# Performance work log

Measured on AMD Instinct MI355X. Metric: run time of the kernel, lower is better.

Reference implementation:

```python
import jax, jax.numpy as jnp
import numpy as np

B, T_IN, IN = 512, 64, 16
HS, OUT = 32, 32          # Seq2Seq hidden_size; decoder output_size == hidden_size
H = HS * 30               # actual GRU state width = 960
T_PRED = 48


def _p(key, shape, scale=0.05):
    return jax.random.normal(key, shape, dtype=jnp.float32) * scale


def setup_inputs() -> dict:
    key = jax.random.key(0)
    ks = jax.random.split(key, 24)
    G = 3 * H
    return {
        "in_data": jax.random.normal(ks[0], (B, T_IN, IN), dtype=jnp.float32),
        "last_location": jax.random.normal(ks[1], (B, 1, HS), dtype=jnp.float32),
        "pred_length": T_PRED,
        # encoder GRU (2 layers)
        "enc_Wih0": _p(ks[2], (G, IN)), "enc_Whh0": _p(ks[3], (G, H)),
        "enc_bih0": _p(ks[4], (G,)), "enc_bhh0": _p(ks[5], (G,)),
        "enc_Wih1": _p(ks[6], (G, H)), "enc_Whh1": _p(ks[7], (G, H)),
        "enc_bih1": _p(ks[8], (G,)), "enc_bhh1": _p(ks[9], (G,)),
        # decoder GRU (2 layers), input size = HS
        "dec_Wih0": _p(ks[10], (G, HS)), "dec_Whh0": _p(ks[11], (G, H)),
        "dec_bih0": _p(ks[12], (G,)), "dec_bhh0": _p(ks[13], (G,)),
        "dec_Wih1": _p(ks[14], (G, H)), "dec_Whh1": _p(ks[15], (G, H)),
        "dec_bih1": _p(ks[16], (G,)), "dec_bhh1": _p(ks[17], (G,)),
        # output projection H -> OUT
        "lin_W": _p(ks[18], (OUT, H)), "lin_b": _p(ks[19], (OUT,)),
    }


def gru_cell(x, h, Wih, Whh, bih, bhh):
    # PyTorch GRU cell convention (gate order: r, z, n)
    gi = x @ Wih.T + bih
    gh = h @ Whh.T + bhh
    ir, iz, inn = jnp.split(gi, 3, axis=-1)
    hr, hz, hn = jnp.split(gh, 3, axis=-1)
    r = jax.nn.sigmoid(ir + hr)
    z = jax.nn.sigmoid(iz + hz)
    n = jnp.tanh(inn + r * hn)
    return (1.0 - z) * n + z * h


def gru_layer(xs, Wih, Whh, bih, bhh):
    # xs: [T, B, in] time-major; zero initial state
    h0 = jnp.zeros((xs.shape[1], Whh.shape[1]), xs.dtype)
    def step(h, x):
        h2 = gru_cell(x, h, Wih, Whh, bih, bhh)
        return h2, h2
    hT, ys = jax.lax.scan(step, h0, xs)
    return ys, hT


def reference(in_data, last_location, pred_length,
              enc_Wih0, enc_Whh0, enc_bih0, enc_bhh0,
              enc_Wih1, enc_Whh1, enc_bih1, enc_bhh1,
              dec_Wih0, dec_Whh0, dec_bih0, dec_bhh0,
              dec_Wih1, dec_Whh1, dec_bih1, dec_bhh1,
              lin_W, lin_b):
    # ---- encoder: 2-layer GRU over in_data ----
    xs = jnp.transpose(in_data, (1, 0, 2))          # [T, B, IN]
    ys0, h0 = gru_layer(xs, enc_Wih0, enc_Whh0, enc_bih0, enc_bhh0)
    ys1, h1 = gru_layer(ys0, enc_Wih1, enc_Whh1, enc_bih1, enc_bhh1)

    x0 = last_location[:, 0, :]                      # [B, HS]

    def dec_step(carry, _):
        hl0, hl1, x = carry
        hl0 = gru_cell(x, hl0, dec_Wih0, dec_Whh0, dec_bih0, dec_bhh0)
        hl1 = gru_cell(hl0, hl1, dec_Wih1, dec_Whh1, dec_bih1, dec_bhh1)
        # dropout is identity in eval mode
        out = hl1 @ lin_W.T + lin_b                  # [B, OUT]
        hcat = jnp.concatenate([hl0, hl1], axis=-1)  # [B, 2H] (layer-major, as permute+view)
        return (hl0, hl1, out), (out, hcat)

    (_, _, _), (outs, hcats) = jax.lax.scan(dec_step, (h0, h1, x0), None, length=pred_length)
    outputs = jnp.transpose(outs, (1, 0, 2))         # [B, T_pred, OUT]
    hidden_outputs = jnp.transpose(hcats, (1, 0, 2)) # [B, T_pred, 2H]
    return outputs, hidden_outputs
```

## Files before the change

### kernel.cpp

```cpp
#include <hip/hip_runtime.h>
#include <cstdint>
#include <cstddef>

typedef __bf16 bf16;
typedef __bf16 bf16x8 __attribute__((ext_vector_type(8)));
typedef float f32x4 __attribute__((ext_vector_type(4)));

static __device__ __forceinline__ f32x4 mfma16(bf16x8 a, bf16x8 b, f32x4 c) {
  return __builtin_amdgcn_mfma_f32_16x16x32_bf16(a, b, c, 0, 0, 0);
}

struct StepArgs {
  const bf16* X;
  const bf16* Hb;
  const bf16* Wt;
  const float* bA;
  const float* bB;
  const float* Hf_prev;
  float* Hf_next;
  bf16* Hb_next;
  float* out_hidden;
  int ldx;
  int KXPAD;
  int Ktot;
  int _pad;
};

__global__ __launch_bounds__(256) void gru_step(StepArgs a0, StepArgs a1) {
  const StepArgs a = (blockIdx.z == 0) ? a0 : a1;
  const int id = blockIdx.x;
  const int gq = id >> 6, bm = (id >> 3) & 7, gr = id & 7;
  const int g = gq * 8 + gr;
  if (g >= 30) return;

  __shared__ bf16 ldsB[2 * 3840];

  const int tid = threadIdx.x;
  const int wv = tid >> 6, lane = tid & 63, col = lane & 15, quad = lane >> 4;
  const int mh = wv & 1, uh = wv >> 1;
  const int Ktot = a.Ktot, KXPAD = a.KXPAD;
  const int nb = tid >> 3, cc = tid & 7;

  const bf16* Wb0 = a.Wt + ((size_t)g * 96 + nb) * Ktot + cc * 4;
  const size_t WrS = (size_t)32 * Ktot;
  char* ldsW = (char*)ldsB + nb * 80 + cc * 8;

  const int rowA = bm * 64 + mh * 32 + col;
  const bf16* Xrow = a.X + (size_t)rowA * a.ldx + quad * 8;
  const bf16* Hrow = a.Hb + (size_t)rowA * 960 + quad * 8 - KXPAD;
  const int ldx16 = 16 * a.ldx;

  const f32x4 z4 = {0.f, 0.f, 0.f, 0.f};
  f32x4 acc[2][3] = {{z4, z4, z4}, {z4, z4, z4}};
  f32x4 ck0 = z4, ck1 = z4;

  uint2 br00, br01, br02, br10, br11, br12;
  bf16x8 ar0, ar1;

#define STAGE0(K) do { br00 = *(const uint2*)(Wb0 + (K)); \
                       br01 = *(const uint2*)(Wb0 + WrS + (K)); \
                       br02 = *(const uint2*)(Wb0 + 2 * WrS + (K)); } while (0)
#define STAGE1(K) do { br10 = *(const uint2*)(Wb0 + (K)); \
                       br11 = *(const uint2*)(Wb0 + WrS + (K)); \
                       br12 = *(const uint2*)(Wb0 + 2 * WrS + (K)); } while (0)
#define LOADA(K) do { int _k = (K); \
    if (_k < KXPAD) { const bf16* _p = Xrow + _k; ar0 = *(const bf16x8*)_p; ar1 = *(const bf16x8*)(_p + ldx16); } \
    else { const bf16* _p = Hrow + _k; ar0 = *(const bf16x8*)_p; ar1 = *(const bf16x8*)(_p + 16 * 960); } } while (0)

  const char* ldsRd = (char*)ldsB + (uh * 16 + col) * 80 + quad * 16;

#define GRU_ITER(PH) do { \
    if (k0 == KXPAD) { ck0 = acc[0][2]; ck1 = acc[1][2]; } \
    char* _d = ldsW + bufoff; \
    *(uint2*)_d = br##PH##0; \
    *(uint2*)(_d + 32 * 80) = br##PH##1; \
    *(uint2*)(_d + 64 * 80) = br##PH##2; \
    bf16x8 am0 = ar0, am1 = ar1; \
    __syncthreads(); \
    { int _k2 = k0 + 64; if (_k2 >= Ktot) _k2 = 0; STAGE##PH(_k2); } \
    { int _kn = k0 + 32; if (_kn >= Ktot) _kn = 0; LOADA(_kn); } \
    const char* _rp = ldsRd + bufoff; \
    _Pragma("unroll") \
    for (int gate = 0; gate < 3; ++gate) { \
      bf16x8 _bf = *(const bf16x8*)(_rp + gate * (32 * 80)); \
      acc[0][gate] = mfma16(am0, _bf, acc[0][gate]); \
      acc[1][gate] = mfma16(am1, _bf, acc[1][gate]); \
    } \
    k0 += 32; bufoff ^= 7680; \
  } while (0)

  STAGE0(0);
  STAGE1(32 < Ktot ? 32 : 0);
  LOADA(0);
  int k0 = 0, bufoff = 0;
  const int T = Ktot >> 5;
  for (int it = 0; it + 2 <= T; it += 2) {
    GRU_ITER(0);
    GRU_ITER(1);
  }
  if (T & 1) { GRU_ITER(0); }

#undef GRU_ITER
#undef STAGE0
#undef STAGE1
#undef LOADA

  const int uu = uh * 16 + col;
  const int u = g * 32 + uu;
  const int gbase = g * 96;
  const float bAr = a.bA[gbase + uu];
  const float bAz = a.bA[gbase + 32 + uu];
  const float bAn = a.bA[gbase + 64 + uu];
  const float bBn = a.bB[gbase + 64 + uu];
#pragma unroll
  for (int mf = 0; mf < 2; ++mf) {
    f32x4 R = acc[mf][0], Z = acc[mf][1], Nf = acc[mf][2];
    f32x4 Nx = mf ? ck1 : ck0;
    const int mbase = bm * 64 + mh * 32 + mf * 16 + quad * 4;
#pragma unroll
    for (int r = 0; r < 4; ++r) {
      const int mm = mbase + r;
      float rg = 1.f / (1.f + __expf(-(R[r] + bAr)));
      float zg = 1.f / (1.f + __expf(-(Z[r] + bAz)));
      float inn = Nx[r] + bAn;
      float hn = (Nf[r] - Nx[r]) + bBn;
      float ng = tanhf(fmaf(rg, hn, inn));
      float hold = a.Hf_prev[(size_t)mm * 960 + u];
      float hnew = fmaf(zg, hold - ng, ng);
      a.Hf_next[(size_t)mm * 960 + u] = hnew;
      a.Hb_next[(size_t)mm * 960 + u] = (bf16)hnew;
      if (a.out_hidden) a.out_hidden[(size_t)mm * 92160 + u] = hnew;
    }
  }
}

__global__ __launch_bounds__(256) void final_linear(const float* __restrict__ hid,
                                                    const bf16* __restrict__ Wb,
                                                    const float* __restrict__ bias,
                                                    float* __restrict__ outp) {
  const int tid = threadIdx.x;
  const int wv = tid >> 6, lane = tid & 63, col = lane & 15, quad = lane >> 4;
  const int row = blockIdx.x * 64 + wv * 16 + col;
  const int b = row / 48, t = row - b * 48;
  const float* arow = hid + (size_t)b * 92160 + (size_t)t * 1920 + 960 + quad * 8;
  const f32x4 z4 = {0.f, 0.f, 0.f, 0.f};
  f32x4 acc0 = z4, acc1 = z4;
  for (int k0 = 0; k0 < 960; k0 += 32) {
    f32x4 x0 = *(const f32x4*)(arow + k0);
    f32x4 x1 = *(const f32x4*)(arow + k0 + 4);
    bf16x8 af;
#pragma unroll
    for (int i = 0; i < 4; ++i) { af[i] = (bf16)x0[i]; af[4 + i] = (bf16)x1[i]; }
    bf16x8 b0 = *(const bf16x8*)(Wb + (size_t)col * 960 + k0 + quad * 8);
    bf16x8 b1 = *(const bf16x8*)(Wb + (size_t)(16 + col) * 960 + k0 + quad * 8);
    acc0 = mfma16(af, b0, acc0);
    acc1 = mfma16(af, b1, acc1);
  }
  const int mbase = blockIdx.x * 64 + wv * 16 + quad * 4;
#pragma unroll
  for (int r = 0; r < 4; ++r) {
    const int mm = mbase + r;
    const int b2 = mm / 48, t2 = mm - b2 * 48;
    float* o = outp + (size_t)b2 * 1536 + (size_t)t2 * 32;
    o[col] = acc0[r] + bias[col];
    o[16 + col] = acc1[r] + bias[16 + col];
  }
}

__global__ void prep_weight(const float* __restrict__ Wih, const float* __restrict__ Whh,
                            bf16* __restrict__ dst, int Kx, int KXPAD, int Ktot) {
  const int total = 2880 * Ktot;
  for (int e = blockIdx.x * blockDim.x + threadIdx.x; e < total; e += gridDim.x * blockDim.x) {
    int n = e / Ktot, k = e - n * Ktot;
    int g = n / 96, loc = n - g * 96, gate = loc >> 5, uu = loc & 31;
    int c = gate * 960 + g * 32 + uu;
    float v;
    if (k < KXPAD) v = (k < Kx) ? Wih[(size_t)c * Kx + k] : 0.f;
    else v = Whh[(size_t)c * 960 + (k - KXPAD)];
    dst[e] = (bf16)v;
  }
}

__global__ void prep_weight_dec0(const float* __restrict__ Wih, const float* __restrict__ Whh,
                                 const float* __restrict__ linW, bf16* __restrict__ dst) {
  const int total = 2880 * 1920;
  for (int e = blockIdx.x * blockDim.x + threadIdx.x; e < total; e += gridDim.x * blockDim.x) {
    int n = e / 1920, k = e - n * 1920;
    int g = n / 96, loc = n - g * 96, gate = loc >> 5, uu = loc & 31;
    int c = gate * 960 + g * 32 + uu;
    float v;
    if (k < 960) {
      float s = 0.f;
      for (int j = 0; j < 32; ++j) s = fmaf(Wih[(size_t)c * 32 + j], linW[(size_t)j * 960 + k], s);
      v = s;
    } else {
      v = Whh[(size_t)c * 960 + (k - 960)];
    }
    dst[e] = (bf16)v;
  }
}

__global__ void prep_bias(const float* __restrict__ bih, const float* __restrict__ bhh,
                          float* __restrict__ bA, float* __restrict__ bB) {
  int n = blockIdx.x * blockDim.x + threadIdx.x;
  if (n >= 2880) return;
  int g = n / 96, loc = n - g * 96, gate = loc >> 5, uu = loc & 31;
  int c = gate * 960 + g * 32 + uu;
  if (gate < 2) { bA[n] = bih[c] + bhh[c]; bB[n] = 0.f; }
  else          { bA[n] = bih[c];          bB[n] = bhh[c]; }
}

__global__ void prep_bias_dec0(const float* __restrict__ bih, const float* __restrict__ bhh,
                               const float* __restrict__ Wih, const float* __restrict__ linb,
                               float* __restrict__ bA, float* __restrict__ bB) {
  int n = blockIdx.x * blockDim.x + threadIdx.x;
  if (n >= 2880) return;
  int g = n / 96, loc = n - g * 96, gate = loc >> 5, uu = loc & 31;
  int c = gate * 960 + g * 32 + uu;
  float bi = bih[c];
  for (int j = 0; j < 32; ++j) bi = fmaf(Wih[(size_t)c * 32 + j], linb[j], bi);
  if (gate < 2) { bA[n] = bi + bhh[c]; bB[n] = 0.f; }
  else          { bA[n] = bi;          bB[n] = bhh[c]; }
}

__global__ void prep_xenc(const float* __restrict__ in_data, bf16* __restrict__ X) {
  int i = blockIdx.x * blockDim.x + threadIdx.x;
  if (i >= 64 * 512 * 32) return;
  int k = i & 31, m = (i >> 5) & 511, t = i >> 14;
  X[i] = (k < 16) ? (bf16)in_data[((size_t)m * 64 + t) * 16 + k] : (bf16)0.f;
}

__global__ void cvt_bf16(const float* __restrict__ s, bf16* __restrict__ d, int n) {
  int i = blockIdx.x * blockDim.x + threadIdx.x;
  if (i < n) d[i] = (bf16)s[i];
}

extern "C" void kernel_launch(void* const* d_in, const int* in_sizes, int n_in,
                              void* d_out, int out_size, void* d_ws, size_t ws_size,
                              hipStream_t stream) {
  (void)in_sizes; (void)n_in; (void)out_size; (void)ws_size;
  const float* in_data = (const float*)d_in[0];
  const float* last_loc = (const float*)d_in[1];
  const float* eWih0 = (const float*)d_in[3];
  const float* eWhh0 = (const float*)d_in[4];
  const float* ebih0 = (const float*)d_in[5];
  const float* ebhh0 = (const float*)d_in[6];
  const float* eWih1 = (const float*)d_in[7];
  const float* eWhh1 = (const float*)d_in[8];
  const float* ebih1 = (const float*)d_in[9];
  const float* ebhh1 = (const float*)d_in[10];
  const float* dWih0 = (const float*)d_in[11];
  const float* dWhh0 = (const float*)d_in[12];
  const float* dbih0 = (const float*)d_in[13];
  const float* dbhh0 = (const float*)d_in[14];
  const float* dWih1 = (const float*)d_in[15];
  const float* dWhh1 = (const float*)d_in[16];
  const float* dbih1 = (const float*)d_in[17];
  const float* dbhh1 = (const float*)d_in[18];
  const float* linW = (const float*)d_in[19];
  const float* linb = (const float*)d_in[20];
  float* outp = (float*)d_out;

  uint8_t* base = (uint8_t*)d_ws;
  size_t off = 0;
  auto alloc = [&](size_t bytes) -> void* {
    void* p = base + off;
    off += (bytes + 255) & ~(size_t)255;
    return p;
  };
  bf16* WtE0 = (bf16*)alloc(2880ull * 992 * 2);
  bf16* WtE1 = (bf16*)alloc(2880ull * 1920 * 2);
  bf16* WtD0a = (bf16*)alloc(2880ull * 992 * 2);
  bf16* WtD0 = (bf16*)alloc(2880ull * 1920 * 2);
  bf16* WtD1 = (bf16*)alloc(2880ull * 1920 * 2);
  bf16* linWb = (bf16*)alloc(32ull * 960 * 2);
  float* bA_e0 = (float*)alloc(2880 * 4); float* bB_e0 = (float*)alloc(2880 * 4);
  float* bA_e1 = (float*)alloc(2880 * 4); float* bB_e1 = (float*)alloc(2880 * 4);
  float* bA_d0a = (float*)alloc(2880 * 4); float* bB_d0a = (float*)alloc(2880 * 4);
  float* bA_d0 = (float*)alloc(2880 * 4); float* bB_d0 = (float*)alloc(2880 * 4);
  float* bA_d1 = (float*)alloc(2880 * 4); float* bB_d1 = (float*)alloc(2880 * 4);
  bf16* Xenc = (bf16*)alloc(64ull * 512 * 32 * 2);
  bf16* Xloc = (bf16*)alloc(512ull * 32 * 2);
  const int HS_ELEMS = 512 * 960;
  float* states = (float*)alloc((size_t)HS_ELEMS * (4 * 4 + 4 * 2));
  float* h0f[2] = {states, states + HS_ELEMS};
  float* h1f[2] = {states + 2 * HS_ELEMS, states + 3 * HS_ELEMS};
  bf16* bstates = (bf16*)(states + 4 * HS_ELEMS);
  bf16* h0b[2] = {bstates, bstates + HS_ELEMS};
  bf16* h1b[2] = {bstates + 2 * HS_ELEMS, bstates + 3 * HS_ELEMS};

  hipMemsetAsync(states, 0, (size_t)HS_ELEMS * (4 * 4 + 4 * 2), stream);
  prep_weight<<<4096, 256, 0, stream>>>(eWih0, eWhh0, WtE0, 16, 32, 992);
  prep_weight<<<8192, 256, 0, stream>>>(eWih1, eWhh1, WtE1, 960, 960, 1920);
  prep_weight<<<4096, 256, 0, stream>>>(dWih0, dWhh0, WtD0a, 32, 32, 992);
  prep_weight_dec0<<<8192, 256, 0, stream>>>(dWih0, dWhh0, linW, WtD0);
  prep_weight<<<8192, 256, 0, stream>>>(dWih1, dWhh1, WtD1, 960, 960, 1920);
  prep_bias<<<12, 256, 0, stream>>>(ebih0, ebhh0, bA_e0, bB_e0);
  prep_bias<<<12, 256, 0, stream>>>(ebih1, ebhh1, bA_e1, bB_e1);
  prep_bias<<<12, 256, 0, stream>>>(dbih0, dbhh0, bA_d0a, bB_d0a);
  prep_bias_dec0<<<12, 256, 0, stream>>>(dbih0, dbhh0, dWih0, linb, bA_d0, bB_d0);
  prep_bias<<<12, 256, 0, stream>>>(dbih1, dbhh1, bA_d1, bB_d1);
  prep_xenc<<<(64 * 512 * 32 + 255) / 256, 256, 0, stream>>>(in_data, Xenc);
  cvt_bf16<<<(512 * 32 + 255) / 256, 256, 0, stream>>>(last_loc, Xloc, 512 * 32);
  cvt_bf16<<<(32 * 960 + 255) / 256, 256, 0, stream>>>(linW, linWb, 32 * 960);

  auto step_args = [](const bf16* X, int ldx, const bf16* Hb, const bf16* Wt,
                      const float* bA, const float* bB, int KXPAD, int Ktot,
                      const float* Hfp, float* Hfn, bf16* Hbn, float* oh) {
    StepArgs s;
    s.X = X; s.ldx = ldx; s.Hb = Hb; s.Wt = Wt; s.bA = bA; s.bB = bB;
    s.KXPAD = KXPAD; s.Ktot = Ktot; s.Hf_prev = Hfp; s.Hf_next = Hfn;
    s.Hb_next = Hbn; s.out_hidden = oh; s._pad = 0;
    return s;
  };

  int p0 = 0, p1 = 0;
  {
    StepArgs s = step_args(Xenc, 32, h0b[p0], WtE0, bA_e0, bB_e0, 32, 992,
                           h0f[p0], h0f[1 - p0], h0b[1 - p0], nullptr);
    gru_step<<<dim3(256, 1, 1), 256, 0, stream>>>(s, s);
    p0 ^= 1;
  }
  for (int t = 1; t < 64; ++t) {
    StepArgs s0 = step_args(Xenc + (size_t)t * 512 * 32, 32, h0b[p0], WtE0, bA_e0, bB_e0, 32, 992,
                            h0f[p0], h0f[1 - p0], h0b[1 - p0], nullptr);
    StepArgs s1 = step_args(h0b[p0], 960, h1b[p1], WtE1, bA_e1, bB_e1, 960, 1920,
                            h1f[p1], h1f[1 - p1], h1b[1 - p1], nullptr);
    gru_step<<<dim3(256, 1, 2), 256, 0, stream>>>(s0, s1);
    p0 ^= 1; p1 ^= 1;
  }
  {
    StepArgs s1 = step_args(h0b[p0], 960, h1b[p1], WtE1, bA_e1, bB_e1, 960, 1920,
                            h1f[p1], h1f[1 - p1], h1b[1 - p1], nullptr);
    gru_step<<<dim3(256, 1, 1), 256, 0, stream>>>(s1, s1);
    p1 ^= 1;
  }
  float* hid = outp + 786432;
  for (int t = 0; t < 48; ++t) {
    StepArgs s0;
    if (t == 0)
      s0 = step_args(Xloc, 32, h0b[p0], WtD0a, bA_d0a, bB_d0a, 32, 992,
                     h0f[p0], h0f[1 - p0], h0b[1 - p0], hid + (size_t)t * 1920);
    else
      s0 = step_args(h1b[p1], 960, h0b[p0], WtD0, bA_d0, bB_d0, 960, 1920,
                     h0f[p0], h0f[1 - p0], h0b[1 - p0], hid + (size_t)t * 1920);
    gru_step<<<dim3(256, 1, 1), 256, 0, stream>>>(s0, s0);
    p0 ^= 1;
    StepArgs s1 = step_args(h0b[p0], 960, h1b[p1], WtD1, bA_d1, bB_d1, 960, 1920,
                            h1f[p1], h1f[1 - p1], h1b[1 - p1], hid + (size_t)t * 1920 + 960);
    gru_step<<<dim3(256, 1, 1), 256, 0, stream>>>(s1, s1);
    p1 ^= 1;
  }
  final_linear<<<384, 256, 0, stream>>>(hid, linWb, linb, outp);
}
```

Baseline: 5.849 ms.

## Process two K-chunks per barrier with deeper prefetch in GRU step kernel

```diff
diff --git a/kernel.cpp b/kernel.cpp
--- a/kernel.cpp
+++ b/kernel.cpp
@@ -33,7 +33,7 @@
   const int g = gq * 8 + gr;
   if (g >= 30) return;
 
-  __shared__ bf16 ldsB[2 * 3840];
+  __shared__ bf16 ldsB[4 * 3840];
 
   const int tid = threadIdx.x;
   const int wv = tid >> 6, lane = tid & 63, col = lane & 15, quad = lane >> 4;
@@ -49,61 +49,6 @@
   const bf16* Xrow = a.X + (size_t)rowA * a.ldx + quad * 8;
   const bf16* Hrow = a.Hb + (size_t)rowA * 960 + quad * 8 - KXPAD;
   const int ldx16 = 16 * a.ldx;
-
-  const f32x4 z4 = {0.f, 0.f, 0.f, 0.f};
-  f32x4 acc[2][3] = {{z4, z4, z4}, {z4, z4, z4}};
-  f32x4 ck0 = z4, ck1 = z4;
-
-  uint2 br00, br01, br02, br10, br11, br12;
-  bf16x8 ar0, ar1;
-
-#define STAGE0(K) do { br00 = *(const uint2*)(Wb0 + (K)); \
-                       br01 = *(const uint2*)(Wb0 + WrS + (K)); \
-                       br02 = *(const uint2*)(Wb0 + 2 * WrS + (K)); } while (0)
-#define STAGE1(K) do { br10 = *(const uint2*)(Wb0 + (K)); \
-                       br11 = *(const uint2*)(Wb0 + WrS + (K)); \
-                       br12 = *(const uint2*)(Wb0 + 2 * WrS + (K)); } while (0)
-#define LOADA(K) do { int _k = (K); \
-    if (_k < KXPAD) { const bf16* _p = Xrow + _k; ar0 = *(const bf16x8*)_p; ar1 = *(const bf16x8*)(_p + ldx16); } \
-    else { const bf16* _p = Hrow + _k; ar0 = *(const bf16x8*)_p; ar1 = *(const bf16x8*)(_p + 16 * 960); } } while (0)
-
-  const char* ldsRd = (char*)ldsB + (uh * 16 + col) * 80 + quad * 16;
-
-#define GRU_ITER(PH) do { \
-    if (k0 == KXPAD) { ck0 = acc[0][2]; ck1 = acc[1][2]; } \
-    char* _d = ldsW + bufoff; \
-    *(uint2*)_d = br##PH##0; \
-    *(uint2*)(_d + 32 * 80) = br##PH##1; \
-    *(uint2*)(_d + 64 * 80) = br##PH##2; \
-    bf16x8 am0 = ar0, am1 = ar1; \
-    __syncthreads(); \
-    { int _k2 = k0 + 64; if (_k2 >= Ktot) _k2 = 0; STAGE##PH(_k2); } \
-    { int _kn = k0 + 32; if (_kn >= Ktot) _kn = 0; LOADA(_kn); } \
-    const char* _rp = ldsRd + bufoff; \
-    _Pragma("unroll") \
-    for (int gate = 0; gate < 3; ++gate) { \
-      bf16x8 _bf = *(const bf16x8*)(_rp + gate * (32 * 80)); \
-      acc[0][gate] = mfma16(am0, _bf, acc[0][gate]); \
-      acc[1][gate] = mfma16(am1, _bf, acc[1][gate]); \
-    } \
-    k0 += 32; bufoff ^= 7680; \
-  } while (0)
-
-  STAGE0(0);
-  STAGE1(32 < Ktot ? 32 : 0);
-  LOADA(0);
-  int k0 = 0, bufoff = 0;
-  const int T = Ktot >> 5;
-  for (int it = 0; it + 2 <= T; it += 2) {
-    GRU_ITER(0);
-    GRU_ITER(1);
-  }
-  if (T & 1) { GRU_ITER(0); }
-
-#undef GRU_ITER
-#undef STAGE0
-#undef STAGE1
-#undef LOADA
 
   const int uu = uh * 16 + col;
   const int u = g * 32 + uu;
@@ -112,11 +57,117 @@
   const float bAz = a.bA[gbase + 32 + uu];
   const float bAn = a.bA[gbase + 64 + uu];
   const float bBn = a.bB[gbase + 64 + uu];
+  const int mb0 = bm * 64 + mh * 32 + quad * 4;
+  float hold[2][4];
+#pragma unroll
+  for (int mf = 0; mf < 2; ++mf)
+#pragma unroll
+    for (int r = 0; r < 4; ++r)
+      hold[mf][r] = a.Hf_prev[(size_t)(mb0 + mf * 16 + r) * 960 + u];
+
+  const f32x4 z4 = {0.f, 0.f, 0.f, 0.f};
+  f32x4 acc[2][3] = {{z4, z4, z4}, {z4, z4, z4}};
+  f32x4 ck0 = z4, ck1 = z4;
+
+  uint2 br0[6], br1[6];
+  bf16x8 ar0[4], ar1[4];
+
+#define STAGEP(PH, K) do { int _ka = (K); int _kb = _ka + 32; if (_kb >= Ktot) _kb = 0; \
+    br##PH[0] = *(const uint2*)(Wb0 + _ka); \
+    br##PH[1] = *(const uint2*)(Wb0 + WrS + _ka); \
+    br##PH[2] = *(const uint2*)(Wb0 + 2 * WrS + _ka); \
+    br##PH[3] = *(const uint2*)(Wb0 + _kb); \
+    br##PH[4] = *(const uint2*)(Wb0 + WrS + _kb); \
+    br##PH[5] = *(const uint2*)(Wb0 + 2 * WrS + _kb); } while (0)
+
+#define LOADA1(D0, D1, KK) do { int _k1 = (KK); \
+    if (_k1 < KXPAD) { const bf16* _p = Xrow + _k1; D0 = *(const bf16x8*)_p; D1 = *(const bf16x8*)(_p + ldx16); } \
+    else { const bf16* _p = Hrow + _k1; D0 = *(const bf16x8*)_p; D1 = *(const bf16x8*)(_p + 16 * 960); } } while (0)
+
+#define LOADAP(PH, K) do { int _ka2 = (K); int _kb2 = _ka2 + 32; if (_kb2 >= Ktot) _kb2 = 0; \
+    LOADA1(ar##PH[0], ar##PH[1], _ka2); LOADA1(ar##PH[2], ar##PH[3], _kb2); } while (0)
+
+  const char* ldsRd = (char*)ldsB + (uh * 16 + col) * 80 + quad * 16;
+
+#define BARRIER() do { \
+    asm volatile("s_waitcnt lgkmcnt(0)" ::: "memory"); \
+    __builtin_amdgcn_s_barrier(); \
+    asm volatile("" ::: "memory"); } while (0)
+
+#define GRU_PAIR(PH) do { \
+    if (k0 == KXPAD) { ck0 = acc[0][2]; ck1 = acc[1][2]; } \
+    char* _d = ldsW + bufoff; \
+    *(uint2*)(_d)               = br##PH[0]; \
+    *(uint2*)(_d + 2560)        = br##PH[1]; \
+    *(uint2*)(_d + 5120)        = br##PH[2]; \
+    *(uint2*)(_d + 7680)        = br##PH[3]; \
+    *(uint2*)(_d + 7680 + 2560) = br##PH[4]; \
+    *(uint2*)(_d + 7680 + 5120) = br##PH[5]; \
+    bf16x8 am0 = ar##PH[0], am1 = ar##PH[1], am2 = ar##PH[2], am3 = ar##PH[3]; \
+    BARRIER(); \
+    { int _k2 = k0 + 128; if (_k2 >= Ktot) _k2 = 0; STAGEP(PH, _k2); LOADAP(PH, _k2); } \
+    const char* _rp = ldsRd + bufoff; \
+    _Pragma("unroll") \
+    for (int gate = 0; gate < 3; ++gate) { \
+      bf16x8 _bf = *(const bf16x8*)(_rp + gate * 2560); \
+      acc[0][gate] = mfma16(am0, _bf, acc[0][gate]); \
+      acc[1][gate] = mfma16(am1, _bf, acc[1][gate]); \
+    } \
+    if (k0 + 32 == KXPAD) { ck0 = acc[0][2]; ck1 = acc[1][2]; } \
+    _Pragma("unroll") \
+    for (int gate = 0; gate < 3; ++gate) { \
+      bf16x8 _bf = *(const bf16x8*)(_rp + 7680 + gate * 2560); \
+      acc[0][gate] = mfma16(am2, _bf, acc[0][gate]); \
+      acc[1][gate] = mfma16(am3, _bf, acc[1][gate]); \
+    } \
+    k0 += 64; bufoff ^= 15360; \
+  } while (0)
+
+#define TAILT(PH) do { \
+    char* _d = ldsW + bufoff; \
+    *(uint2*)(_d)        = br##PH[0]; \
+    *(uint2*)(_d + 2560) = br##PH[1]; \
+    *(uint2*)(_d + 5120) = br##PH[2]; \
+    bf16x8 am0 = ar##PH[0], am1 = ar##PH[1]; \
+    BARRIER(); \
+    const char* _rp = ldsRd + bufoff; \
+    _Pragma("unroll") \
+    for (int gate = 0; gate < 3; ++gate) { \
+      bf16x8 _bf = *(const bf16x8*)(_rp + gate * 2560); \
+      acc[0][gate] = mfma16(am0, _bf, acc[0][gate]); \
+      acc[1][gate] = mfma16(am1, _bf, acc[1][gate]); \
+    } \
+  } while (0)
+
+  STAGEP(0, 0);
+  STAGEP(1, 64);
+  LOADAP(0, 0);
+  LOADAP(1, 64);
+  int k0 = 0, bufoff = 0;
+  const int T32 = Ktot >> 5;
+  const int npair = T32 >> 1;
+  for (int it = 0; it + 2 <= npair; it += 2) {
+    GRU_PAIR(0);
+    GRU_PAIR(1);
+  }
+  if (npair & 1) { GRU_PAIR(0); }
+  if (T32 & 1) {
+    if (k0 == KXPAD) { ck0 = acc[0][2]; ck1 = acc[1][2]; }
+    if (npair & 1) TAILT(1); else TAILT(0);
+  }
+
+#undef GRU_PAIR
+#undef TAILT
+#undef BARRIER
+#undef STAGEP
+#undef LOADAP
+#undef LOADA1
+
 #pragma unroll
   for (int mf = 0; mf < 2; ++mf) {
     f32x4 R = acc[mf][0], Z = acc[mf][1], Nf = acc[mf][2];
     f32x4 Nx = mf ? ck1 : ck0;
-    const int mbase = bm * 64 + mh * 32 + mf * 16 + quad * 4;
+    const int mbase = mb0 + mf * 16;
 #pragma unroll
     for (int r = 0; r < 4; ++r) {
       const int mm = mbase + r;
@@ -125,8 +176,7 @@
       float inn = Nx[r] + bAn;
       float hn = (Nf[r] - Nx[r]) + bBn;
       float ng = tanhf(fmaf(rg, hn, inn));
-      float hold = a.Hf_prev[(size_t)mm * 960 + u];
-      float hnew = fmaf(zg, hold - ng, ng);
+      float hnew = fmaf(zg, hold[mf][r] - ng, ng);
       a.Hf_next[(size_t)mm * 960 + u] = hnew;
       a.Hb_next[(size_t)mm * 960 + u] = (bf16)hnew;
       if (a.out_hidden) a.out_hidden[(size_t)mm * 92160 + u] = hnew;
```

After: 5.018 ms. 14.2% less time.

## Replace LDS-staged weight tiles with deep register-prefetched direct global loads

Applied to the files above, without the earlier changes.

```diff
diff --git a/kernel.cpp b/kernel.cpp
--- a/kernel.cpp
+++ b/kernel.cpp
@@ -33,77 +33,19 @@
   const int g = gq * 8 + gr;
   if (g >= 30) return;
 
-  __shared__ bf16 ldsB[2 * 3840];
-
   const int tid = threadIdx.x;
   const int wv = tid >> 6, lane = tid & 63, col = lane & 15, quad = lane >> 4;
   const int mh = wv & 1, uh = wv >> 1;
   const int Ktot = a.Ktot, KXPAD = a.KXPAD;
-  const int nb = tid >> 3, cc = tid & 7;
-
-  const bf16* Wb0 = a.Wt + ((size_t)g * 96 + nb) * Ktot + cc * 4;
-  const size_t WrS = (size_t)32 * Ktot;
-  char* ldsW = (char*)ldsB + nb * 80 + cc * 8;
 
   const int rowA = bm * 64 + mh * 32 + col;
   const bf16* Xrow = a.X + (size_t)rowA * a.ldx + quad * 8;
   const bf16* Hrow = a.Hb + (size_t)rowA * 960 + quad * 8 - KXPAD;
   const int ldx16 = 16 * a.ldx;
 
-  const f32x4 z4 = {0.f, 0.f, 0.f, 0.f};
-  f32x4 acc[2][3] = {{z4, z4, z4}, {z4, z4, z4}};
-  f32x4 ck0 = z4, ck1 = z4;
-
-  uint2 br00, br01, br02, br10, br11, br12;
-  bf16x8 ar0, ar1;
-
-#define STAGE0(K) do { br00 = *(const uint2*)(Wb0 + (K)); \
-                       br01 = *(const uint2*)(Wb0 + WrS + (K)); \
-                       br02 = *(const uint2*)(Wb0 + 2 * WrS + (K)); } while (0)
-#define STAGE1(K) do { br10 = *(const uint2*)(Wb0 + (K)); \
-                       br11 = *(const uint2*)(Wb0 + WrS + (K)); \
-                       br12 = *(const uint2*)(Wb0 + 2 * WrS + (K)); } while (0)
-#define LOADA(K) do { int _k = (K); \
-    if (_k < KXPAD) { const bf16* _p = Xrow + _k; ar0 = *(const bf16x8*)_p; ar1 = *(const bf16x8*)(_p + ldx16); } \
-    else { const bf16* _p = Hrow + _k; ar0 = *(const bf16x8*)_p; ar1 = *(const bf16x8*)(_p + 16 * 960); } } while (0)
-
-  const char* ldsRd = (char*)ldsB + (uh * 16 + col) * 80 + quad * 16;
-
-#define GRU_ITER(PH) do { \
-    if (k0 == KXPAD) { ck0 = acc[0][2]; ck1 = acc[1][2]; } \
-    char* _d = ldsW + bufoff; \
-    *(uint2*)_d = br##PH##0; \
-    *(uint2*)(_d + 32 * 80) = br##PH##1; \
-    *(uint2*)(_d + 64 * 80) = br##PH##2; \
-    bf16x8 am0 = ar0, am1 = ar1; \
-    __syncthreads(); \
-    { int _k2 = k0 + 64; if (_k2 >= Ktot) _k2 = 0; STAGE##PH(_k2); } \
-    { int _kn = k0 + 32; if (_kn >= Ktot) _kn = 0; LOADA(_kn); } \
-    const char* _rp = ldsRd + bufoff; \
-    _Pragma("unroll") \
-    for (int gate = 0; gate < 3; ++gate) { \
-      bf16x8 _bf = *(const bf16x8*)(_rp + gate * (32 * 80)); \
-      acc[0][gate] = mfma16(am0, _bf, acc[0][gate]); \
-      acc[1][gate] = mfma16(am1, _bf, acc[1][gate]); \
-    } \
-    k0 += 32; bufoff ^= 7680; \
-  } while (0)
-
-  STAGE0(0);
-  STAGE1(32 < Ktot ? 32 : 0);
-  LOADA(0);
-  int k0 = 0, bufoff = 0;
-  const int T = Ktot >> 5;
-  for (int it = 0; it + 2 <= T; it += 2) {
-    GRU_ITER(0);
-    GRU_ITER(1);
-  }
-  if (T & 1) { GRU_ITER(0); }
-
-#undef GRU_ITER
-#undef STAGE0
-#undef STAGE1
-#undef LOADA
+  const bf16* Wr0 = a.Wt + (size_t)(g * 96 + uh * 16 + col) * Ktot + quad * 8;
+  const bf16* Wr1 = Wr0 + (size_t)32 * Ktot;
+  const bf16* Wr2 = Wr0 + (size_t)64 * Ktot;
 
   const int uu = uh * 16 + col;
   const int u = g * 32 + uu;
@@ -112,11 +54,80 @@
   const float bAz = a.bA[gbase + 32 + uu];
   const float bAn = a.bA[gbase + 64 + uu];
   const float bBn = a.bB[gbase + 64 + uu];
+  const int mb0 = bm * 64 + mh * 32 + quad * 4;
+  float hold[2][4];
+#pragma unroll
+  for (int mf = 0; mf < 2; ++mf)
+#pragma unroll
+    for (int r = 0; r < 4; ++r)
+      hold[mf][r] = a.Hf_prev[(size_t)(mb0 + mf * 16 + r) * 960 + u];
+
+  const f32x4 z4 = {0.f, 0.f, 0.f, 0.f};
+  f32x4 acc[2][3] = {{z4, z4, z4}, {z4, z4, z4}};
+  f32x4 ck0 = z4, ck1 = z4;
+
+  bf16x8 aR[8][2];
+  bf16x8 bR[8][3];
+
+#define LOADT(P, K) do { int _k = (K); \
+    if (_k < KXPAD) { const bf16* _p = Xrow + _k; \
+      aR[P][0] = *(const bf16x8*)_p; aR[P][1] = *(const bf16x8*)(_p + ldx16); } \
+    else { const bf16* _p = Hrow + _k; \
+      aR[P][0] = *(const bf16x8*)_p; aR[P][1] = *(const bf16x8*)(_p + 16 * 960); } \
+    bR[P][0] = *(const bf16x8*)(Wr0 + _k); \
+    bR[P][1] = *(const bf16x8*)(Wr1 + _k); \
+    bR[P][2] = *(const bf16x8*)(Wr2 + _k); } while (0)
+
+#define CONS(P, KC) do { \
+    if ((KC) == KXPAD) { ck0 = acc[0][2]; ck1 = acc[1][2]; } \
+    _Pragma("unroll") \
+    for (int gf = 0; gf < 3; ++gf) { \
+      acc[0][gf] = mfma16(aR[P][0], bR[P][gf], acc[0][gf]); \
+      acc[1][gf] = mfma16(aR[P][1], bR[P][gf], acc[1][gf]); \
+    } } while (0)
+
+  LOADT(0, 0);   LOADT(1, 32);  LOADT(2, 64);  LOADT(3, 96);
+  LOADT(4, 128); LOADT(5, 160); LOADT(6, 192); LOADT(7, 224);
+
+  int k0 = 0;
+  for (; k0 + 512 <= Ktot; k0 += 256) {
+    CONS(0, k0);       LOADT(0, k0 + 256);
+    CONS(1, k0 + 32);  LOADT(1, k0 + 288);
+    CONS(2, k0 + 64);  LOADT(2, k0 + 320);
+    CONS(3, k0 + 96);  LOADT(3, k0 + 352);
+    CONS(4, k0 + 128); LOADT(4, k0 + 384);
+    CONS(5, k0 + 160); LOADT(5, k0 + 416);
+    CONS(6, k0 + 192); LOADT(6, k0 + 448);
+    CONS(7, k0 + 224); LOADT(7, k0 + 480);
+  }
+  if (((Ktot >> 5) & 7) == 4) {
+    CONS(0, k0);       LOADT(0, k0 + 256);
+    CONS(1, k0 + 32);  LOADT(1, k0 + 288);
+    CONS(2, k0 + 64);  LOADT(2, k0 + 320);
+    CONS(3, k0 + 96);  LOADT(3, k0 + 352);
+    CONS(4, k0 + 128); CONS(5, k0 + 160); CONS(6, k0 + 192); CONS(7, k0 + 224);
+    CONS(0, k0 + 256); CONS(1, k0 + 288); CONS(2, k0 + 320); CONS(3, k0 + 352);
+  } else {
+    CONS(0, k0);       LOADT(0, k0 + 256);
+    CONS(1, k0 + 32);  LOADT(1, k0 + 288);
+    CONS(2, k0 + 64);  LOADT(2, k0 + 320);
+    CONS(3, k0 + 96);  LOADT(3, k0 + 352);
+    CONS(4, k0 + 128); LOADT(4, k0 + 384);
+    CONS(5, k0 + 160); LOADT(5, k0 + 416);
+    CONS(6, k0 + 192); LOADT(6, k0 + 448);
+    CONS(7, k0 + 224);
+    CONS(0, k0 + 256); CONS(1, k0 + 288); CONS(2, k0 + 320); CONS(3, k0 + 352);
+    CONS(4, k0 + 384); CONS(5, k0 + 416); CONS(6, k0 + 448);
+  }
+
+#undef CONS
+#undef LOADT
+
 #pragma unroll
   for (int mf = 0; mf < 2; ++mf) {
     f32x4 R = acc[mf][0], Z = acc[mf][1], Nf = acc[mf][2];
     f32x4 Nx = mf ? ck1 : ck0;
-    const int mbase = bm * 64 + mh * 32 + mf * 16 + quad * 4;
+    const int mbase = mb0 + mf * 16;
 #pragma unroll
     for (int r = 0; r < 4; ++r) {
       const int mm = mbase + r;
@@ -125,8 +136,7 @@
       float inn = Nx[r] + bAn;
       float hn = (Nf[r] - Nx[r]) + bBn;
       float ng = tanhf(fmaf(rg, hn, inn));
-      float hold = a.Hf_prev[(size_t)mm * 960 + u];
-      float hnew = fmaf(zg, hold - ng, ng);
+      float hnew = fmaf(zg, hold[mf][r] - ng, ng);
       a.Hf_next[(size_t)mm * 960 + u] = hnew;
       a.Hb_next[(size_t)mm * 960 + u] = (bf16)hnew;
       if (a.out_hidden) a.out_hidden[(size_t)mm * 92160 + u] = hnew;
```

After: 7.189 ms. 22.9% more time.
